# Kernel optimization log

Measured on AMD Instinct MI355X. Metric: run time of the kernel, lower is better.

The kernel has to match this reference:

```python
import jax, jax.numpy as jnp
import numpy as np

LN_EPS = 1e-5


def _layernorm(h, gamma, beta):
    mu = jnp.mean(h, axis=-1, keepdims=True)
    var = jnp.var(h, axis=-1, keepdims=True)
    return (h - mu) * jax.lax.rsqrt(var + LN_EPS) * gamma + beta


def _simple_attention(q, k, v):
    # DIFFormer 'simple' kernel, num_heads=1: global-Frobenius-normalized q,k,
    # linear attention numerator + uniform component, denominator + N.
    n = q.shape[0]
    qs = q / jnp.linalg.norm(q)            # [N, M]
    ks = k / jnp.linalg.norm(k)            # [N, M]
    kvs = jnp.einsum('lm,ld->md', ks, v)   # [M, D]
    num = jnp.einsum('nm,md->nd', qs, kvs) + jnp.sum(v, axis=0)  # [N, D]
    den = jnp.einsum('nm,m->n', qs, jnp.sum(ks, axis=0)) + jnp.asarray(n, q.dtype)
    return num / den[:, None]


def reference(x, edge_index, W1, b1, Wq, bq, Wk, bk, gamma, beta, alpha, Wr, br, wgt):
    n = x.shape[0]
    row, col = edge_index[0], edge_index[1]
    # symmetric GCN normalization (degree of destination index, as in DIFFormer)
    deg = jax.ops.segment_sum(jnp.ones_like(col, dtype=x.dtype), col, num_segments=n)
    inv_sqrt = jnp.where(deg > 0, 1.0 / jnp.sqrt(deg), 0.0)
    w_edge = inv_sqrt[col] * inv_sqrt[row]  # [E]

    def gcn_conv(v):
        # out[i] = sum_{e: col[e]==i} w[e] * v[row[e]]
        return jax.ops.segment_sum(w_edge[:, None] * v[row], col, num_segments=n)

    def conv(h):
        q = h @ Wq + bq
        k = h @ Wk + bk
        v = h                              # use_weight=False -> value = source input
        return _simple_attention(q, k, v) + gcn_conv(v)

    R = jax.nn.relu(x @ W1 + b1)           # [N, H]
    Ts = [R]
    for _ in range(3):                      # three calls of the SAME shared conv
        Rn = conv(R)
        R = alpha * Rn + (1.0 - alpha) * R  # residual blend
        R = _layernorm(R, gamma, beta)      # shared LayerNorm
        Ts.append(R)

    # multi-head linear readout + learned weighted sum (dropout = identity in eval)
    res = jnp.stack([Ts[i] @ Wr[i] + br[i] for i in range(4)], axis=0)  # [4, N]
    out = jnp.einsum('i,in->n', wgt, res)[:, None]                       # [N, 1]
    return out


def setup_inputs():
    key = jax.random.key(0)
    ks = jax.random.split(key, 8)
    N, E, F_IN, H = 100000, 3200000, 58, 256
    x = jax.random.normal(ks[0], (N, F_IN), dtype=jnp.float32)
    edge_index = jax.random.randint(ks[1], (2, E), 0, N, dtype=jnp.int32)
    s_in = 1.0 / np.sqrt(F_IN)
    s_h = 1.0 / np.sqrt(H)
    return {
        'x': x,
        'edge_index': edge_index,
        'W1': jax.random.normal(ks[2], (F_IN, H), dtype=jnp.float32) * s_in,
        'b1': jnp.zeros((H,), jnp.float32),
        'Wq': jax.random.normal(ks[3], (H, H), dtype=jnp.float32) * s_h,
        'bq': jnp.zeros((H,), jnp.float32),
        'Wk': jax.random.normal(ks[4], (H, H), dtype=jnp.float32) * s_h,
        'bk': jnp.zeros((H,), jnp.float32),
        'gamma': jnp.ones((H,), jnp.float32),
        'beta': jnp.zeros((H,), jnp.float32),
        'alpha': jnp.float32(0.5),
        'Wr': jax.random.normal(ks[5], (4, H), dtype=jnp.float32) * s_h,
        'br': jnp.zeros((4,), jnp.float32),
        'wgt': jnp.array([0.5, 0.5, 0.5, 0.5], jnp.float32),
    }
```

## Files before the change

### kernel.cpp

```cpp
#include <hip/hip_runtime.h>

#define H 256
#define FIN 58
#define LN_EPS 1e-5f
#define ROWS_PB 544
#define EPB 8192
#define SBW 11

typedef __bf16 bf16x8 __attribute__((ext_vector_type(8)));
typedef float f32x16 __attribute__((ext_vector_type(16)));
typedef float f32x2 __attribute__((ext_vector_type(2)));

union FragU {
  ushort u[8];
  bf16x8 v;
};


__device__ __forceinline__ float wave_sum(float v) {
#pragma unroll
  for (int off = 1; off < 64; off <<= 1) v += __shfl_xor(v, off, 64);
  return v;
}

__device__ __forceinline__ float block_sum(float v, volatile float* red) {
  const int tid = threadIdx.x;
  v = wave_sum(v);
  __syncthreads();
  if ((tid & 63) == 0) red[tid >> 6] = v;
  __syncthreads();
  return red[0] + red[1] + red[2] + red[3];
}

__device__ __forceinline__ ushort f2bf(float f) {
  unsigned u = __float_as_uint(f);
  unsigned r = (u + 0x7FFFu + ((u >> 16) & 1u)) >> 16;
  return (ushort)r;
}

__device__ __forceinline__ float bf2f(ushort u) {
  return __uint_as_float((unsigned)u << 16);
}

#if __has_builtin(__builtin_amdgcn_cvt_pk_fp8_f32) && __has_builtin(__builtin_amdgcn_cvt_pk_f32_fp8)
__device__ __forceinline__ unsigned pack_fp8x4(float a, float b, float c, float d) {
  int v = 0;
  v = __builtin_amdgcn_cvt_pk_fp8_f32(a, b, v, false);
  v = __builtin_amdgcn_cvt_pk_fp8_f32(c, d, v, true);
  return (unsigned)v;
}
__device__ __forceinline__ void unpack_fp8x4_acc(float* acc, unsigned v) {
  f32x2 lo = __builtin_amdgcn_cvt_pk_f32_fp8((int)v, false);
  f32x2 hi = __builtin_amdgcn_cvt_pk_f32_fp8((int)v, true);
  acc[0] += lo[0]; acc[1] += lo[1]; acc[2] += hi[0]; acc[3] += hi[1];
}
#else
__device__ __forceinline__ unsigned char f2e4m3_1(float f) {
  unsigned u = __float_as_uint(f);
  unsigned s = (u >> 31) << 7;
  float a = fabsf(f);
  if (a >= 448.0f) return (unsigned char)(s | 0x7E);
  if (a < 0.0009765625f) return (unsigned char)s;
  int e;
  float m = frexpf(a, &e);
  int E = e - 1 + 7;
  if (E >= 1) {
    int mm = (int)rintf((m * 2.0f - 1.0f) * 8.0f);
    if (mm == 8) { mm = 0; E++; }
    return (unsigned char)(s | (E << 3) | mm);
  }
  int mm = (int)rintf(a * 512.0f);
  if (mm > 7) return (unsigned char)(s | (1 << 3));
  return (unsigned char)(s | mm);
}
__device__ __forceinline__ unsigned pack_fp8x4(float a, float b, float c, float d) {
  return (unsigned)f2e4m3_1(a) | ((unsigned)f2e4m3_1(b) << 8) |
         ((unsigned)f2e4m3_1(c) << 16) | ((unsigned)f2e4m3_1(d) << 24);
}
__device__ __forceinline__ float e4m3f_1(unsigned v) {
  int s = (v >> 7) & 1, E = (v >> 3) & 15, m = v & 7;
  float mag = E ? ldexpf(1.0f + m * 0.125f, E - 7) : ldexpf((float)m, -9);
  return s ? -mag : mag;
}
__device__ __forceinline__ void unpack_fp8x4_acc(float* acc, unsigned v) {
  acc[0] += e4m3f_1(v & 255);
  acc[1] += e4m3f_1((v >> 8) & 255);
  acc[2] += e4m3f_1((v >> 16) & 255);
  acc[3] += e4m3f_1(v >> 24);
}
#endif


__global__ __launch_bounds__(512) void k_b1(const int* __restrict__ row,
                                            const int* __restrict__ col,
                                            unsigned* __restrict__ breg,
                                            int* __restrict__ gcnt,
                                            int cap2, int E, int nsb) {
  __shared__ unsigned stage[EPB];
  __shared__ int lh[65], lbase[65], lcur[64], gclaim[64];
  const int tid = threadIdx.x;
  const int e0 = blockIdx.x * EPB;
  const int cnt = min(EPB, E - e0);
  if (tid < 64) lh[tid] = 0;
  __syncthreads();
  for (int i = tid; i < cnt; i += 512) atomicAdd(&lh[col[e0 + i] >> SBW], 1);
  __syncthreads();
  if (tid == 0) {
    int acc = 0;
    for (int b = 0; b < nsb; b++) { lbase[b] = acc; acc += lh[b]; }
    lbase[nsb] = acc;
  }
  __syncthreads();
  if (tid < nsb) {
    gclaim[tid] = atomicAdd(&gcnt[tid], lh[tid]);
    lcur[tid] = lbase[tid];
  }
  __syncthreads();
  for (int i = tid; i < cnt; i += 512) {
    int c = col[e0 + i];
    int b = c >> SBW;
    int s = atomicAdd(&lcur[b], 1);
    stage[s] = ((unsigned)row[e0 + i] << SBW) | (unsigned)(c & ((1 << SBW) - 1));
  }
  __syncthreads();
  for (int i = tid; i < cnt; i += 512) {
    int lo = 0, hi = nsb;
    while (hi - lo > 1) {
      int mid = (lo + hi) >> 1;
      if (lbase[mid] <= i) lo = mid; else hi = mid;
    }
    int off = gclaim[lo] + (i - lbase[lo]);
    if (off < cap2) breg[(size_t)lo * cap2 + off] = stage[i];
  }
}

__global__ __launch_bounds__(512) void k_degB2(const unsigned* __restrict__ breg,
                                               const int* __restrict__ gcnt, int cap2,
                                               int* __restrict__ deg, int N) {
  __shared__ int lcnt[1 << SBW];
  const int b = blockIdx.x, tid = threadIdx.x, base = b << SBW;
  for (int i = tid; i < (1 << SBW); i += 512) lcnt[i] = 0;
  __syncthreads();
  const int cnt = min(gcnt[b], cap2);
  const unsigned* p = breg + (size_t)b * cap2;
  for (int i = tid; i < cnt; i += 512) atomicAdd(&lcnt[p[i] & ((1 << SBW) - 1)], 1);
  __syncthreads();
  for (int i = tid; i < (1 << SBW); i += 512) {
    int d = base + i;
    if (d < N) deg[d] = lcnt[i];
  }
}

__global__ __launch_bounds__(512) void k_b2(const unsigned* __restrict__ breg,
                                            const int* __restrict__ gcnt, int cap2,
                                            const int* __restrict__ offs16,
                                            int* __restrict__ eb, int N) {
  __shared__ int loffs[1 << SBW];
  __shared__ int lcur[1 << SBW];
  const int b = blockIdx.x, tid = threadIdx.x, base = b << SBW;
  for (int i = tid; i < (1 << SBW); i += 512) {
    int d = base + i;
    loffs[i] = (d < N) ? offs16[d] : 0;
    lcur[i] = 0;
  }
  __syncthreads();
  const int cnt = min(gcnt[b], cap2);
  const unsigned* p = breg + (size_t)b * cap2;
  for (int i = tid; i < cnt; i += 512) {
    unsigned rc = p[i];
    int lc = rc & ((1 << SBW) - 1);
    int slot = atomicAdd(&lcur[lc], 1);
    eb[loffs[lc] + slot] = (int)(rc >> SBW);
  }
  __syncthreads();
  for (int i = tid; i < (1 << SBW); i += 512) {
    int d = base + i;
    if (d < N) {
      int c = lcur[i];
      int pad = (c + 15) & ~15;
      int o = loffs[i];
      for (int j = c; j < pad; j++) eb[o + j] = N;
    }
  }
}

__global__ void k_invsqrt(const int* __restrict__ deg, float* __restrict__ invs, int N) {
  int i = blockIdx.x * 256 + threadIdx.x;
  if (i < N) {
    int d = deg[i];
    invs[i] = (d > 0) ? (1.0f / sqrtf((float)d)) : 0.0f;
  }
}

__global__ __launch_bounds__(1024) void k_scan1(const int* __restrict__ deg,
                                                int* __restrict__ offs16,
                                                int* __restrict__ bsum, int N) {
  __shared__ int buf[1024];
  const int tid = threadIdx.x;
  const int gid = blockIdx.x * 1024 + tid;
  int v = (gid < N) ? ((deg[gid] + 15) & ~15) : 0;
  buf[tid] = v;
  __syncthreads();
  for (int off = 1; off < 1024; off <<= 1) {
    int x = (tid >= off) ? buf[tid - off] : 0;
    __syncthreads();
    buf[tid] += x;
    __syncthreads();
  }
  if (gid < N) offs16[gid] = buf[tid] - v;
  if (tid == 1023) bsum[blockIdx.x] = buf[1023];
}

__global__ __launch_bounds__(1024) void k_scan2(int* __restrict__ bsum, int nb) {
  __shared__ int buf[1024];
  const int tid = threadIdx.x;
  int v = (tid < nb) ? bsum[tid] : 0;
  buf[tid] = v;
  __syncthreads();
  for (int off = 1; off < 1024; off <<= 1) {
    int x = (tid >= off) ? buf[tid - off] : 0;
    __syncthreads();
    buf[tid] += x;
    __syncthreads();
  }
  if (tid < nb) bsum[tid] = buf[tid] - v;
}

__global__ void k_scan3(int* __restrict__ offs16, const int* __restrict__ bsum, int N) {
  int i = blockIdx.x * 256 + threadIdx.x;
  if (i < N) offs16[i] += bsum[i >> 10];
}

__global__ void k_tofp8(const ushort* __restrict__ Rb, const float* __restrict__ invs,
                        unsigned* __restrict__ Rf8, int total8) {
  for (int i = blockIdx.x * 256 + threadIdx.x; i < total8; i += gridDim.x * 256) {
    float s = invs[i >> 5];
    int4 v = ((const int4*)Rb)[i];
    const ushort* pu = (const ushort*)&v;
    unsigned lo = pack_fp8x4(bf2f(pu[0]) * s, bf2f(pu[1]) * s, bf2f(pu[2]) * s, bf2f(pu[3]) * s);
    unsigned hi = pack_fp8x4(bf2f(pu[4]) * s, bf2f(pu[5]) * s, bf2f(pu[6]) * s, bf2f(pu[7]) * s);
    ((uint2*)Rf8)[i] = make_uint2(lo, hi);
  }
}

__global__ void k_prep(const float* __restrict__ Wq, const float* __restrict__ Wk,
                       const float* __restrict__ bq, const float* __restrict__ bk,
                       float* __restrict__ P, float* __restrict__ Q, float* __restrict__ K2,
                       float* __restrict__ pb, float* __restrict__ qb,
                       float* __restrict__ wb, float* __restrict__ kb,
                       float* __restrict__ sconst) {
  __shared__ float red[4];
  const int b = blockIdx.x, tid = threadIdx.x;
  if (b < 768) {
    const int f = b & 255, which = b >> 8;
    const float* A = (which == 2) ? Wk : Wq;
    const float* Bm = (which == 1) ? Wq : Wk;
    float acc = 0.0f;
    for (int m = 0; m < H; m++) acc = fmaf(A[f * H + m], Bm[tid * H + m], acc);
    float* D = (which == 0) ? P : ((which == 1) ? Q : K2);
    D[f * H + tid] = acc;
  } else {
    float a1 = 0, a2 = 0, a3 = 0, a4 = 0;
    for (int m = 0; m < H; m++) {
      float wqv = Wq[tid * H + m], wkv = Wk[tid * H + m];
      a1 = fmaf(wqv, bk[m], a1);
      a2 = fmaf(wqv, bq[m], a2);
      a3 = fmaf(wkv, bq[m], a3);
      a4 = fmaf(wkv, bk[m], a4);
    }
    pb[tid] = a1; qb[tid] = a2; wb[tid] = a3; kb[tid] = a4;
    float c0 = block_sum(bq[tid] * bk[tid], red);
    float c1 = block_sum(bq[tid] * bq[tid], red);
    float c2 = block_sum(bk[tid] * bk[tid], red);
    if (tid == 0) { sconst[0] = c0; sconst[1] = c1; sconst[2] = c2; }
  }
}

__global__ void k_fc1(const float* __restrict__ x, const float* __restrict__ W1,
                      const float* __restrict__ b1, const float* __restrict__ Wr,
                      const float* __restrict__ br, const float* __restrict__ wgt,
                      ushort* __restrict__ R0, float* __restrict__ out, int N) {
  __shared__ __align__(16) float lx[16 * FIN];
  __shared__ float red2[4][16];
  const int tid = threadIdx.x;
  const int n0 = blockIdx.x * 16;
  for (int idx = tid; idx < 16 * FIN / 4; idx += 256)
    ((float4*)lx)[idx] = ((const float4*)(x + (size_t)n0 * FIN))[idx];
  __syncthreads();
  float acc[16];
  const float bias = b1[tid];
#pragma unroll
  for (int r = 0; r < 16; r++) acc[r] = bias;
  for (int f = 0; f < FIN; f++) {
    float wv = W1[f * H + tid];
#pragma unroll
    for (int r = 0; r < 16; r++) acc[r] = fmaf(lx[r * FIN + f], wv, acc[r]);
  }
  const float wr0 = Wr[tid];
#pragma unroll
  for (int r = 0; r < 16; r++) {
    acc[r] = fmaxf(acc[r], 0.0f);
    int n = n0 + r;
    if (n < N) R0[(size_t)n * H + tid] = f2bf(acc[r]);
  }
#pragma unroll
  for (int r = 0; r < 16; r++) {
    float s = wave_sum(acc[r] * wr0);
    if ((tid & 63) == 0) red2[tid >> 6][r] = s;
  }
  __syncthreads();
  if (tid < 16) {
    int n = n0 + tid;
    if (n < N)
      out[n] = wgt[0] * (red2[0][tid] + red2[1][tid] + red2[2][tid] + red2[3][tid] + br[0]);
  }
}

__global__ __launch_bounds__(512, 2) void k_Gm(const ushort* __restrict__ Rb,
                                               float* __restrict__ Gslab,
                                               float* __restrict__ vsum, int N) {
  __shared__ ushort sb[2][32 * 256];
  const int tid = threadIdx.x;
  const int lane = tid & 63;
  const int wid = tid >> 6;
  const int wrow = (wid & 1) * 128;
  const int wcol = (wid >> 1) * 64;
  const int l31 = lane & 31;
  const int lhi = lane >> 5;

  const int rowbase = blockIdx.x * ROWS_PB;
  const int nrows = min(ROWS_PB, N - rowbase);
  const int nch = (nrows + 31) >> 5;

  const int sk = tid >> 4;
  const int c0 = (tid & 15) * 16;

  f32x16 acc[4][2];
#pragma unroll
  for (int s = 0; s < 4; s++)
#pragma unroll
    for (int t = 0; t < 2; t++)
#pragma unroll
      for (int e = 0; e < 16; e++) acc[s][t][e] = 0.0f;

  float csum[16];
#pragma unroll
  for (int i = 0; i < 16; i++) csum[i] = 0.0f;

  int4 ld[2];

  auto load_chunk = [&](int ch) {
    int g = rowbase + ch * 32 + sk;
    const int4* src = (const int4*)(Rb + (size_t)g * H + c0);
    ld[0] = (g < N) ? src[0] : make_int4(0, 0, 0, 0);
    ld[1] = (g < N) ? src[1] : make_int4(0, 0, 0, 0);
  };

  auto write_chunk = [&](int buf) {
    const int swz = (sk & 3) << 4;
#pragma unroll
    for (int i = 0; i < 2; i++) {
      *(int4*)&sb[buf][sk * 256 + ((c0 + 8 * i) ^ swz)] = ld[i];
      const ushort* pu = (const ushort*)&ld[i];
#pragma unroll
      for (int j = 0; j < 8; j++) csum[8 * i + j] += bf2f(pu[j]);
    }
  };

  auto compute = [&](int buf) {
#pragma unroll
    for (int ks = 0; ks < 2; ks++) {
      const int kb = ks * 16 + lhi * 8;
      FragU fr[6];
#pragma unroll
      for (int s = 0; s < 6; s++) {
        const int cbase = (s < 4) ? (wrow + 32 * s + l31) : (wcol + 32 * (s - 4) + l31);
#pragma unroll
        for (int j = 0; j < 8; j++)
          fr[s].u[j] = sb[buf][(kb + j) * 256 + (cbase ^ ((j & 3) << 4))];
      }
#pragma unroll
      for (int s = 0; s < 4; s++)
#pragma unroll
        for (int t = 0; t < 2; t++)
          acc[s][t] = __builtin_amdgcn_mfma_f32_32x32x16_bf16(fr[s].v, fr[4 + t].v,
                                                              acc[s][t], 0, 0, 0);
    }
  };

  if (nch > 0) {
    load_chunk(0);
    write_chunk(0);
    __syncthreads();
    int cur = 0;
    for (int c = 0; c < nch; c++) {
      if (c + 1 < nch) load_chunk(c + 1);
      compute(cur);
      if (c + 1 < nch) write_chunk(cur ^ 1);
      __syncthreads();
      cur ^= 1;
    }
  }

  float* Gs = Gslab + (size_t)blockIdx.x * 65536;
#pragma unroll
  for (int s = 0; s < 4; s++)
#pragma unroll
    for (int t = 0; t < 2; t++) {
      const int n0 = wcol + 32 * t + l31;
#pragma unroll
      for (int r = 0; r < 16; r++) {
        const int row = wrow + 32 * s + (r & 3) + 8 * (r >> 2) + 4 * lhi;
        Gs[row * 256 + n0] = acc[s][t][r];
      }
    }

  float* fl = (float*)sb;
#pragma unroll
  for (int j = 0; j < 16; j++) fl[sk * 256 + c0 + j] = csum[j];
  __syncthreads();
  if (tid < 256) {
    float s = 0.0f;
    for (int r = 0; r < 32; r++) s += fl[r * 256 + tid];
    atomicAdd(&vsum[tid], s);
  }
}

__global__ void k_Gr(const float* __restrict__ Gslab, float* __restrict__ G, int nslab) {
  const int i = blockIdx.x * 256 + threadIdx.x;
  float s0 = 0, s1 = 0, s2 = 0, s3 = 0;
  int b = 0;
  for (; b + 3 < nslab; b += 4) {
    s0 += Gslab[(size_t)b * 65536 + i];
    s1 += Gslab[(size_t)(b + 1) * 65536 + i];
    s2 += Gslab[(size_t)(b + 2) * 65536 + i];
    s3 += Gslab[(size_t)(b + 3) * 65536 + i];
  }
  float s = s0 + s1 + s2 + s3;
  for (; b < nslab; b++) s += Gslab[(size_t)b * 65536 + i];
  G[i] = s;
}

__global__ void k_small(const float* __restrict__ G, const float* __restrict__ vsum,
                        const float* __restrict__ P, const float* __restrict__ pb,
                        const float* __restrict__ wb, const float* __restrict__ sconst,
                        const float* __restrict__ Q, const float* __restrict__ K2,
                        ushort* __restrict__ Mt, float* __restrict__ cvec,
                        float* __restrict__ dvec, float* __restrict__ scal, int N) {
  __shared__ float red[4];
  const int b = blockIdx.x, tid = threadIdx.x;
  if (b < 256) {
    float acc = 0.0f;
    for (int m = 0; m < H; m++) acc = fmaf(P[b * H + m], G[m * H + tid], acc);
    Mt[(size_t)tid * H + b] = f2bf(acc + pb[b] * vsum[tid]);
  } else if (b == 256) {
    float acc = 0.0f;
    for (int f = 0; f < H; f++) acc = fmaf(wb[f], G[f * H + tid], acc);
    cvec[tid] = acc + sconst[0] * vsum[tid];
  } else if (b == 257) {
    float acc = 0.0f;
    for (int m = 0; m < H; m++) acc = fmaf(P[tid * H + m], vsum[m], acc);
    dvec[tid] = acc + (float)N * pb[tid];
  } else if (b < 274) {
    int base = (b - 258) * 4096 + tid;
    float a = 0.0f;
    for (int j = 0; j < 16; j++) a = fmaf(G[base + j * 256], Q[base + j * 256], a);
    a = block_sum(a, red);
    if (tid == 0) atomicAdd(&scal[0], a);
  } else {
    int base = (b - 274) * 4096 + tid;
    float a = 0.0f;
    for (int j = 0; j < 16; j++) a = fmaf(G[base + j * 256], K2[base + j * 256], a);
    a = block_sum(a, red);
    if (tid == 0) atomicAdd(&scal[1], a);
  }
}

__global__ void k_final(const float* __restrict__ vsum, const float* __restrict__ qb,
                        const float* __restrict__ kb, const float* __restrict__ wb,
                        const float* __restrict__ sconst, float* __restrict__ scal, int N) {
  __shared__ float red[4];
  const int tid = threadIdx.x;
  float s1 = block_sum(qb[tid] * vsum[tid], red);
  float s2 = block_sum(kb[tid] * vsum[tid], red);
  float s3 = block_sum(wb[tid] * vsum[tid], red);
  if (tid == 0) {
    float sq = scal[0] + 2.0f * s1 + (float)N * sconst[1];
    float sk = scal[1] + 2.0f * s2 + (float)N * sconst[2];
    scal[2] = 1.0f / (sqrtf(sq) * sqrtf(sk));
    scal[3] = s3 + (float)N * sconst[0];
  }
}

__global__ __launch_bounds__(512) void k_N(const ushort* __restrict__ Rb,
                                           const ushort* __restrict__ Mt,
                                           ushort* __restrict__ numb, int N) {
  const int tid = threadIdx.x;
  const int lane = tid & 63;
  const int wid = tid >> 6;
  const int l31 = lane & 31;
  const int lhi = lane >> 5;
  const int wrow = (wid & 3) * 32;
  const int wcol = (wid >> 2) * 128;
  const int rowbase = blockIdx.x * 128;

  f32x16 acc[4];
#pragma unroll
  for (int t = 0; t < 4; t++)
#pragma unroll
    for (int e = 0; e < 16; e++) acc[t][e] = 0.0f;

  const ushort* aptr = Rb + (size_t)(rowbase + wrow + l31) * H;

  for (int kc = 0; kc < 16; kc++) {
    const int kb = kc * 16 + lhi * 8;
    FragU fa;
    *(int4*)fa.u = *(const int4*)(aptr + kb);
    FragU fb0, fb1, fb2, fb3;
    *(int4*)fb0.u = *(const int4*)(Mt + (size_t)(wcol + 0 + l31) * H + kb);
    *(int4*)fb1.u = *(const int4*)(Mt + (size_t)(wcol + 32 + l31) * H + kb);
    *(int4*)fb2.u = *(const int4*)(Mt + (size_t)(wcol + 64 + l31) * H + kb);
    *(int4*)fb3.u = *(const int4*)(Mt + (size_t)(wcol + 96 + l31) * H + kb);
    acc[0] = __builtin_amdgcn_mfma_f32_32x32x16_bf16(fa.v, fb0.v, acc[0], 0, 0, 0);
    acc[1] = __builtin_amdgcn_mfma_f32_32x32x16_bf16(fa.v, fb1.v, acc[1], 0, 0, 0);
    acc[2] = __builtin_amdgcn_mfma_f32_32x32x16_bf16(fa.v, fb2.v, acc[2], 0, 0, 0);
    acc[3] = __builtin_amdgcn_mfma_f32_32x32x16_bf16(fa.v, fb3.v, acc[3], 0, 0, 0);
  }

#pragma unroll
  for (int t = 0; t < 4; t++) {
    const int col = wcol + 32 * t + l31;
#pragma unroll
    for (int r = 0; r < 16; r++) {
      const int row = rowbase + wrow + (r & 3) + 8 * (r >> 2) + 4 * lhi;
      if (row < N) numb[(size_t)row * H + col] = f2bf(acc[t][r]);
    }
  }
}

__global__ __launch_bounds__(256) void k_C(
    const ushort* __restrict__ Rb, ushort* __restrict__ Rnext,
    const ushort* __restrict__ numb, const unsigned* __restrict__ Rf8,
    const int* __restrict__ eb, const float* __restrict__ invs,
    const float* __restrict__ cvec, const float* __restrict__ dvec,
    const float* __restrict__ vsum, const float* __restrict__ scal,
    const int* __restrict__ offs16, const int* __restrict__ deg,
    const float* __restrict__ alphap, const float* __restrict__ gamma,
    const float* __restrict__ beta, const float* __restrict__ Wr,
    const float* __restrict__ br, const float* __restrict__ wgt,
    float* __restrict__ out, int N, int layer, int last) {
  const int tid = threadIdx.x, lane = tid & 63, wv = tid >> 6;
  const int d0 = lane * 4;
  const int n0 = blockIdx.x * 32 + wv * 8;

  const float invn = scal[2], denc = scal[3];
  const float al = alphap[0], om = 1.0f - al;
  const float4 dv = *(const float4*)&dvec[d0];
  const float4 cv = *(const float4*)&cvec[d0];
  const float4 vs = *(const float4*)&vsum[d0];
  const float4 gm = *(const float4*)&gamma[d0];
  const float4 bt = *(const float4*)&beta[d0];
  const float4 wr = *(const float4*)&Wr[layer * H + d0];
  const float wl = wgt[layer], bl = br[layer];

  for (int r = 0; r < 8; r++) {
    const int n = n0 + r;
    if (n >= N) break;
    const ushort4 ro = *(const ushort4*)&Rb[(size_t)n * H + d0];
    const ushort4 no = *(const ushort4*)&numb[(size_t)n * H + d0];
    const float old0 = bf2f(ro.x), old1 = bf2f(ro.y), old2 = bf2f(ro.z), old3 = bf2f(ro.w);

    float p = old0 * dv.x + old1 * dv.y + old2 * dv.z + old3 * dv.w;
    p = wave_sum(p);
    const float rden = 1.0f / ((p + denc) * invn + (float)N);

    float a[4] = {0.0f, 0.0f, 0.0f, 0.0f};
    const int st = offs16[n];
    const int nb = (deg[n] + 15) >> 4;
    const int4* pe = (const int4*)(eb + st);
    for (int b = 0; b < nb; b++, pe += 4) {
      int4 q0 = pe[0], q1 = pe[1], q2 = pe[2], q3 = pe[3];
      unsigned g[16];
      g[0] = Rf8[((size_t)q0.x << 6) + lane];
      g[1] = Rf8[((size_t)q0.y << 6) + lane];
      g[2] = Rf8[((size_t)q0.z << 6) + lane];
      g[3] = Rf8[((size_t)q0.w << 6) + lane];
      g[4] = Rf8[((size_t)q1.x << 6) + lane];
      g[5] = Rf8[((size_t)q1.y << 6) + lane];
      g[6] = Rf8[((size_t)q1.z << 6) + lane];
      g[7] = Rf8[((size_t)q1.w << 6) + lane];
      g[8] = Rf8[((size_t)q2.x << 6) + lane];
      g[9] = Rf8[((size_t)q2.y << 6) + lane];
      g[10] = Rf8[((size_t)q2.z << 6) + lane];
      g[11] = Rf8[((size_t)q2.w << 6) + lane];
      g[12] = Rf8[((size_t)q3.x << 6) + lane];
      g[13] = Rf8[((size_t)q3.y << 6) + lane];
      g[14] = Rf8[((size_t)q3.z << 6) + lane];
      g[15] = Rf8[((size_t)q3.w << 6) + lane];
#pragma unroll
      for (int i = 0; i < 16; i++) unpack_fp8x4_acc(a, g[i]);
    }
    const float sn = invs[n];

    float hv0 = al * (((bf2f(no.x) + cv.x) * invn + vs.x) * rden + a[0] * sn) + om * old0;
    float hv1 = al * (((bf2f(no.y) + cv.y) * invn + vs.y) * rden + a[1] * sn) + om * old1;
    float hv2 = al * (((bf2f(no.z) + cv.z) * invn + vs.z) * rden + a[2] * sn) + om * old2;
    float hv3 = al * (((bf2f(no.w) + cv.w) * invn + vs.w) * rden + a[3] * sn) + om * old3;

    float s = wave_sum(hv0 + hv1 + hv2 + hv3);
    float mu = s * (1.0f / H);
    float s2 = wave_sum(hv0 * hv0 + hv1 * hv1 + hv2 * hv2 + hv3 * hv3);
    float var = s2 * (1.0f / H) - mu * mu;
    float rs = rsqrtf(var + LN_EPS);
    float y0 = (hv0 - mu) * rs * gm.x + bt.x;
    float y1 = (hv1 - mu) * rs * gm.y + bt.y;
    float y2 = (hv2 - mu) * rs * gm.z + bt.z;
    float y3 = (hv3 - mu) * rs * gm.w + bt.w;
    if (!last) {
      ushort4 o;
      o.x = f2bf(y0); o.y = f2bf(y1); o.z = f2bf(y2); o.w = f2bf(y3);
      *(ushort4*)&Rnext[(size_t)n * H + d0] = o;
    }
    float rp = wave_sum(y0 * wr.x + y1 * wr.y + y2 * wr.z + y3 * wr.w);
    if (lane == 0) out[n] += wl * (rp + bl);
  }
}


extern "C" void kernel_launch(void* const* d_in, const int* in_sizes, int n_in,
                              void* d_out, int out_size, void* d_ws, size_t ws_size,
                              hipStream_t stream) {
  const float* x = (const float*)d_in[0];
  const int* ei = (const int*)d_in[1];
  const float* W1 = (const float*)d_in[2];
  const float* b1 = (const float*)d_in[3];
  const float* Wq = (const float*)d_in[4];
  const float* bq = (const float*)d_in[5];
  const float* Wk = (const float*)d_in[6];
  const float* bk = (const float*)d_in[7];
  const float* gamma = (const float*)d_in[8];
  const float* beta = (const float*)d_in[9];
  const float* alphap = (const float*)d_in[10];
  const float* Wr = (const float*)d_in[11];
  const float* br = (const float*)d_in[12];
  const float* wgt = (const float*)d_in[13];
  float* out = (float*)d_out;

  const int N = in_sizes[0] / FIN;
  const int E = in_sizes[1] / 2;
  const int* row = ei;
  const int* col = ei + E;

  char* w = (char*)d_ws;
  auto alloc = [&](size_t bytes) -> char* {
    char* p = w;
    w += (bytes + 255) & ~(size_t)255;
    return p;
  };
  const size_t RB = (size_t)(N + 128) * H * sizeof(ushort);
  ushort* Rb0 = (ushort*)alloc(RB);
  ushort* Rb1 = (ushort*)alloc(RB);
  ushort* numb = (ushort*)alloc(RB);
  unsigned* Rf8 = (unsigned*)alloc((size_t)(N + 1) * 64 * sizeof(unsigned));
  ushort* Mt = (ushort*)alloc(H * H * sizeof(ushort));
  float* G = (float*)alloc(H * H * sizeof(float));
  float* vsum = (float*)alloc(1024);
  float* scal = (float*)alloc(256);
  float* cvec = (float*)alloc(1024);
  float* dvec = (float*)alloc(1024);
  float* P = (float*)alloc(H * H * sizeof(float));
  float* Q = (float*)alloc(H * H * sizeof(float));
  float* K2 = (float*)alloc(H * H * sizeof(float));
  float* pb = (float*)alloc(1024);
  float* qb = (float*)alloc(1024);
  float* wb = (float*)alloc(1024);
  float* kb = (float*)alloc(1024);
  float* sconst = (float*)alloc(256);
  int* deg = (int*)alloc((size_t)N * 4);
  float* invs = (float*)alloc((size_t)N * 4);
  int* offs16 = (int*)alloc((size_t)(N + 1) * 4);
  int* bsum = (int*)alloc(1024 * 4);
  int* gcnt = (int*)alloc(64 * 4);
  size_t EPAD = (size_t)E + 16 * (size_t)N;
  EPAD = (EPAD + 3) & ~(size_t)3;
  int* eb = (int*)alloc(EPAD * sizeof(int));

  const int NSB = (N + (1 << SBW) - 1) >> SBW;
  int cap2 = (E / (NSB > 0 ? NSB : 1)) * 2 + 4096;
  cap2 = (cap2 + 3) & ~3;
  unsigned* breg = (unsigned*)Rb1;
  float* Gslab = (float*)numb;

  hipMemsetAsync(gcnt, 0, 64 * 4, stream);
  hipMemsetAsync(Rf8 + (size_t)N * 64, 0, 64 * sizeof(unsigned), stream);

  const int gN = (N + 255) / 256;
  const int nblk = (N + 1023) / 1024;
  const int nbB1 = (E + EPB - 1) / EPB;
  k_b1<<<nbB1, 512, 0, stream>>>(row, col, breg, gcnt, cap2, E, NSB);
  k_degB2<<<NSB, 512, 0, stream>>>(breg, gcnt, cap2, deg, N);
  k_invsqrt<<<gN, 256, 0, stream>>>(deg, invs, N);
  k_scan1<<<nblk, 1024, 0, stream>>>(deg, offs16, bsum, N);
  k_scan2<<<1, 1024, 0, stream>>>(bsum, nblk);
  k_scan3<<<gN, 256, 0, stream>>>(offs16, bsum, N);
  k_b2<<<NSB, 512, 0, stream>>>(breg, gcnt, cap2, offs16, eb, N);
  k_prep<<<769, 256, 0, stream>>>(Wq, Wk, bq, bk, P, Q, K2, pb, qb, wb, kb, sconst);
  const int gRows16 = (N + 15) / 16;
  k_fc1<<<gRows16, 256, 0, stream>>>(x, W1, b1, Wr, br, wgt, Rb0, out, N);

  const int nbG = (N + ROWS_PB - 1) / ROWS_PB;
  const int nbN = (N + 127) / 128;
  const int gRows32 = (N + 31) / 32;
  const int total8 = N * (H / 8);
  ushort* Rc = Rb0;
  ushort* Rn = Rb1;
  for (int it = 1; it <= 3; ++it) {
    hipMemsetAsync(vsum, 0, 1024 + 256, stream);
    k_Gm<<<nbG, 512, 0, stream>>>(Rc, Gslab, vsum, N);
    k_Gr<<<256, 256, 0, stream>>>(Gslab, G, nbG);
    k_small<<<290, 256, 0, stream>>>(G, vsum, P, pb, wb, sconst, Q, K2, Mt, cvec, dvec, scal, N);
    k_final<<<1, 256, 0, stream>>>(vsum, qb, kb, wb, sconst, scal, N);
    k_tofp8<<<2048, 256, 0, stream>>>(Rc, invs, Rf8, total8);
    k_N<<<nbN, 512, 0, stream>>>(Rc, Mt, numb, N);
    k_C<<<gRows32, 256, 0, stream>>>(Rc, Rn, numb, Rf8, eb, invs, cvec, dvec, vsum, scal,
                                     offs16, deg, alphap, gamma, beta, Wr, br, wgt, out,
                                     N, it, (it == 3) ? 1 : 0);
    ushort* t = Rc; Rc = Rn; Rn = t;
  }
}
```

Before: 1.248 ms.

## Fuse fp8 conversion into Gram kernel, store bf16 slabs, widen gather per lane

Removes the separate fp8 conversion kernel by packing the scaled fp8 copy of R inside k_Gm while the chunk is already in registers. Partial Gram slabs are stored as bf16 instead of fp32, halving the slab traffic read by k_Gr, and ROWS_PB drops so more blocks (and slabs) are launched. The combine kernel now processes two rows per wave with 8 features per lane and 8-byte gathers, halving reduction width. Bf16 partial Gram sums lose precision, and the larger slab count adds reduction work.

```diff
diff --git a/kernel.cpp b/kernel.cpp
--- a/kernel.cpp
+++ b/kernel.cpp
@@ -3,7 +3,7 @@
 #define H 256
 #define FIN 58
 #define LN_EPS 1e-5f
-#define ROWS_PB 544
+#define ROWS_PB 384
 #define EPB 8192
 #define SBW 11
 
@@ -20,6 +20,12 @@
 __device__ __forceinline__ float wave_sum(float v) {
 #pragma unroll
   for (int off = 1; off < 64; off <<= 1) v += __shfl_xor(v, off, 64);
+  return v;
+}
+
+__device__ __forceinline__ float half_sum(float v) {
+#pragma unroll
+  for (int off = 1; off < 32; off <<= 1) v += __shfl_xor(v, off, 64);
   return v;
 }
 
@@ -49,10 +55,9 @@
   v = __builtin_amdgcn_cvt_pk_fp8_f32(c, d, v, true);
   return (unsigned)v;
 }
-__device__ __forceinline__ void unpack_fp8x4_acc(float* acc, unsigned v) {
-  f32x2 lo = __builtin_amdgcn_cvt_pk_f32_fp8((int)v, false);
-  f32x2 hi = __builtin_amdgcn_cvt_pk_f32_fp8((int)v, true);
-  acc[0] += lo[0]; acc[1] += lo[1]; acc[2] += hi[0]; acc[3] += hi[1];
+__device__ __forceinline__ void unpack_fp8x2_acc(f32x2& lo, f32x2& hi, unsigned v) {
+  lo += __builtin_amdgcn_cvt_pk_f32_fp8((int)v, false);
+  hi += __builtin_amdgcn_cvt_pk_f32_fp8((int)v, true);
 }
 #else
 __device__ __forceinline__ unsigned char f2e4m3_1(float f) {
@@ -82,11 +87,11 @@
   float mag = E ? ldexpf(1.0f + m * 0.125f, E - 7) : ldexpf((float)m, -9);
   return s ? -mag : mag;
 }
-__device__ __forceinline__ void unpack_fp8x4_acc(float* acc, unsigned v) {
-  acc[0] += e4m3f_1(v & 255);
-  acc[1] += e4m3f_1((v >> 8) & 255);
-  acc[2] += e4m3f_1((v >> 16) & 255);
-  acc[3] += e4m3f_1(v >> 24);
+__device__ __forceinline__ void unpack_fp8x2_acc(f32x2& lo, f32x2& hi, unsigned v) {
+  lo[0] += e4m3f_1(v & 255);
+  lo[1] += e4m3f_1((v >> 8) & 255);
+  hi[0] += e4m3f_1((v >> 16) & 255);
+  hi[1] += e4m3f_1(v >> 24);
 }
 #endif
 
@@ -229,18 +234,6 @@
 __global__ void k_scan3(int* __restrict__ offs16, const int* __restrict__ bsum, int N) {
   int i = blockIdx.x * 256 + threadIdx.x;
   if (i < N) offs16[i] += bsum[i >> 10];
-}
-
-__global__ void k_tofp8(const ushort* __restrict__ Rb, const float* __restrict__ invs,
-                        unsigned* __restrict__ Rf8, int total8) {
-  for (int i = blockIdx.x * 256 + threadIdx.x; i < total8; i += gridDim.x * 256) {
-    float s = invs[i >> 5];
-    int4 v = ((const int4*)Rb)[i];
-    const ushort* pu = (const ushort*)&v;
-    unsigned lo = pack_fp8x4(bf2f(pu[0]) * s, bf2f(pu[1]) * s, bf2f(pu[2]) * s, bf2f(pu[3]) * s);
-    unsigned hi = pack_fp8x4(bf2f(pu[4]) * s, bf2f(pu[5]) * s, bf2f(pu[6]) * s, bf2f(pu[7]) * s);
-    ((uint2*)Rf8)[i] = make_uint2(lo, hi);
-  }
 }
 
 __global__ void k_prep(const float* __restrict__ Wq, const float* __restrict__ Wk,
@@ -317,7 +310,9 @@
 }
 
 __global__ __launch_bounds__(512, 2) void k_Gm(const ushort* __restrict__ Rb,
-                                               float* __restrict__ Gslab,
+                                               const float* __restrict__ invs,
+                                               ushort* __restrict__ Gslab,
+                                               unsigned* __restrict__ Rf8,
                                                float* __restrict__ vsum, int N) {
   __shared__ ushort sb[2][32 * 256];
   const int tid = threadIdx.x;
@@ -356,15 +351,24 @@
     ld[1] = (g < N) ? src[1] : make_int4(0, 0, 0, 0);
   };
 
-  auto write_chunk = [&](int buf) {
+  auto write_chunk = [&](int ch, int buf) {
+    int g = rowbase + ch * 32 + sk;
     const int swz = (sk & 3) << 4;
+    const float sc = (g < N) ? invs[g] : 0.0f;
+    unsigned w8[4];
 #pragma unroll
     for (int i = 0; i < 2; i++) {
       *(int4*)&sb[buf][sk * 256 + ((c0 + 8 * i) ^ swz)] = ld[i];
       const ushort* pu = (const ushort*)&ld[i];
 #pragma unroll
       for (int j = 0; j < 8; j++) csum[8 * i + j] += bf2f(pu[j]);
-    }
+      w8[2 * i] = pack_fp8x4(bf2f(pu[0]) * sc, bf2f(pu[1]) * sc,
+                             bf2f(pu[2]) * sc, bf2f(pu[3]) * sc);
+      w8[2 * i + 1] = pack_fp8x4(bf2f(pu[4]) * sc, bf2f(pu[5]) * sc,
+                                 bf2f(pu[6]) * sc, bf2f(pu[7]) * sc);
+    }
+    if (g < N)
+      *(uint4*)&Rf8[(size_t)g * 64 + (c0 >> 2)] = make_uint4(w8[0], w8[1], w8[2], w8[3]);
   };
 
   auto compute = [&](int buf) {
@@ -390,28 +394,28 @@
 
   if (nch > 0) {
     load_chunk(0);
-    write_chunk(0);
+    write_chunk(0, 0);
     __syncthreads();
     int cur = 0;
     for (int c = 0; c < nch; c++) {
       if (c + 1 < nch) load_chunk(c + 1);
       compute(cur);
-      if (c + 1 < nch) write_chunk(cur ^ 1);
+      if (c + 1 < nch) write_chunk(c + 1, cur ^ 1);
       __syncthreads();
       cur ^= 1;
     }
   }
 
-  float* Gs = Gslab + (size_t)blockIdx.x * 65536;
+  ushort* Gs = Gslab + (size_t)blockIdx.x * 65536;
 #pragma unroll
   for (int s = 0; s < 4; s++)
 #pragma unroll
     for (int t = 0; t < 2; t++) {
-      const int n0 = wcol + 32 * t + l31;
+      const int n0c = wcol + 32 * t + l31;
 #pragma unroll
       for (int r = 0; r < 16; r++) {
         const int row = wrow + 32 * s + (r & 3) + 8 * (r >> 2) + 4 * lhi;
-        Gs[row * 256 + n0] = acc[s][t][r];
+        Gs[row * 256 + n0c] = f2bf(acc[s][t][r]);
       }
     }
 
@@ -426,18 +430,18 @@
   }
 }
 
-__global__ void k_Gr(const float* __restrict__ Gslab, float* __restrict__ G, int nslab) {
+__global__ void k_Gr(const ushort* __restrict__ Gslab, float* __restrict__ G, int nslab) {
   const int i = blockIdx.x * 256 + threadIdx.x;
   float s0 = 0, s1 = 0, s2 = 0, s3 = 0;
   int b = 0;
   for (; b + 3 < nslab; b += 4) {
-    s0 += Gslab[(size_t)b * 65536 + i];
-    s1 += Gslab[(size_t)(b + 1) * 65536 + i];
-    s2 += Gslab[(size_t)(b + 2) * 65536 + i];
-    s3 += Gslab[(size_t)(b + 3) * 65536 + i];
+    s0 += bf2f(Gslab[(size_t)b * 65536 + i]);
+    s1 += bf2f(Gslab[(size_t)(b + 1) * 65536 + i]);
+    s2 += bf2f(Gslab[(size_t)(b + 2) * 65536 + i]);
+    s3 += bf2f(Gslab[(size_t)(b + 3) * 65536 + i]);
   }
   float s = s0 + s1 + s2 + s3;
-  for (; b < nslab; b++) s += Gslab[(size_t)b * 65536 + i];
+  for (; b < nslab; b++) s += bf2f(Gslab[(size_t)b * 65536 + i]);
   G[i] = s;
 }
 
@@ -550,79 +554,97 @@
     const float* __restrict__ br, const float* __restrict__ wgt,
     float* __restrict__ out, int N, int layer, int last) {
   const int tid = threadIdx.x, lane = tid & 63, wv = tid >> 6;
-  const int d0 = lane * 4;
+  const int half = lane >> 5, hl = lane & 31;
+  const int d0 = hl * 8;
   const int n0 = blockIdx.x * 32 + wv * 8;
 
   const float invn = scal[2], denc = scal[3];
   const float al = alphap[0], om = 1.0f - al;
-  const float4 dv = *(const float4*)&dvec[d0];
-  const float4 cv = *(const float4*)&cvec[d0];
-  const float4 vs = *(const float4*)&vsum[d0];
-  const float4 gm = *(const float4*)&gamma[d0];
-  const float4 bt = *(const float4*)&beta[d0];
-  const float4 wr = *(const float4*)&Wr[layer * H + d0];
+  const float4 dvA = *(const float4*)&dvec[d0];
+  const float4 dvB = *(const float4*)&dvec[d0 + 4];
+  const float4 cvA = *(const float4*)&cvec[d0];
+  const float4 cvB = *(const float4*)&cvec[d0 + 4];
+  const float4 vsA = *(const float4*)&vsum[d0];
+  const float4 vsB = *(const float4*)&vsum[d0 + 4];
+  const float4 gmA = *(const float4*)&gamma[d0];
+  const float4 gmB = *(const float4*)&gamma[d0 + 4];
+  const float4 btA = *(const float4*)&beta[d0];
+  const float4 btB = *(const float4*)&beta[d0 + 4];
+  const float4 wrA = *(const float4*)&Wr[layer * H + d0];
+  const float4 wrB = *(const float4*)&Wr[layer * H + d0 + 4];
   const float wl = wgt[layer], bl = br[layer];
 
-  for (int r = 0; r < 8; r++) {
-    const int n = n0 + r;
-    if (n >= N) break;
-    const ushort4 ro = *(const ushort4*)&Rb[(size_t)n * H + d0];
-    const ushort4 no = *(const ushort4*)&numb[(size_t)n * H + d0];
-    const float old0 = bf2f(ro.x), old1 = bf2f(ro.y), old2 = bf2f(ro.z), old3 = bf2f(ro.w);
-
-    float p = old0 * dv.x + old1 * dv.y + old2 * dv.z + old3 * dv.w;
-    p = wave_sum(p);
+  for (int r = 0; r < 4; r++) {
+    const int n = n0 + r * 2 + half;
+    const bool valid = n < N;
+    const int ns = valid ? n : 0;
+
+    const int4 rv = *(const int4*)&Rb[(size_t)ns * H + d0];
+    const int4 nv = *(const int4*)&numb[(size_t)ns * H + d0];
+    const ushort* rp = (const ushort*)&rv;
+    const ushort* np = (const ushort*)&nv;
+    float old[8], num[8];
+#pragma unroll
+    for (int j = 0; j < 8; j++) { old[j] = bf2f(rp[j]); num[j] = bf2f(np[j]); }
+
+    float p = old[0] * dvA.x + old[1] * dvA.y + old[2] * dvA.z + old[3] * dvA.w +
+              old[4] * dvB.x + old[5] * dvB.y + old[6] * dvB.z + old[7] * dvB.w;
+    p = half_sum(p);
     const float rden = 1.0f / ((p + denc) * invn + (float)N);
 
-    float a[4] = {0.0f, 0.0f, 0.0f, 0.0f};
-    const int st = offs16[n];
-    const int nb = (deg[n] + 15) >> 4;
+    f32x2 a01 = {0.f, 0.f}, a23 = {0.f, 0.f}, a45 = {0.f, 0.f}, a67 = {0.f, 0.f};
+    const int st = offs16[ns];
+    const int nbch = valid ? ((deg[ns] + 15) >> 4) : 0;
     const int4* pe = (const int4*)(eb + st);
-    for (int b = 0; b < nb; b++, pe += 4) {
+    const int woff = hl * 2;
+    for (int b = 0; b < nbch; b++, pe += 4) {
       int4 q0 = pe[0], q1 = pe[1], q2 = pe[2], q3 = pe[3];
-      unsigned g[16];
-      g[0] = Rf8[((size_t)q0.x << 6) + lane];
-      g[1] = Rf8[((size_t)q0.y << 6) + lane];
-      g[2] = Rf8[((size_t)q0.z << 6) + lane];
-      g[3] = Rf8[((size_t)q0.w << 6) + lane];
-      g[4] = Rf8[((size_t)q1.x << 6) + lane];
-      g[5] = Rf8[((size_t)q1.y << 6) + lane];
-      g[6] = Rf8[((size_t)q1.z << 6) + lane];
-      g[7] = Rf8[((size_t)q1.w << 6) + lane];
-      g[8] = Rf8[((size_t)q2.x << 6) + lane];
-      g[9] = Rf8[((size_t)q2.y << 6) + lane];
-      g[10] = Rf8[((size_t)q2.z << 6) + lane];
-      g[11] = Rf8[((size_t)q2.w << 6) + lane];
-      g[12] = Rf8[((size_t)q3.x << 6) + lane];
-      g[13] = Rf8[((size_t)q3.y << 6) + lane];
-      g[14] = Rf8[((size_t)q3.z << 6) + lane];
-      g[15] = Rf8[((size_t)q3.w << 6) + lane];
-#pragma unroll
-      for (int i = 0; i < 16; i++) unpack_fp8x4_acc(a, g[i]);
-    }
-    const float sn = invs[n];
-
-    float hv0 = al * (((bf2f(no.x) + cv.x) * invn + vs.x) * rden + a[0] * sn) + om * old0;
-    float hv1 = al * (((bf2f(no.y) + cv.y) * invn + vs.y) * rden + a[1] * sn) + om * old1;
-    float hv2 = al * (((bf2f(no.z) + cv.z) * invn + vs.z) * rden + a[2] * sn) + om * old2;
-    float hv3 = al * (((bf2f(no.w) + cv.w) * invn + vs.w) * rden + a[3] * sn) + om * old3;
-
-    float s = wave_sum(hv0 + hv1 + hv2 + hv3);
-    float mu = s * (1.0f / H);
-    float s2 = wave_sum(hv0 * hv0 + hv1 * hv1 + hv2 * hv2 + hv3 * hv3);
-    float var = s2 * (1.0f / H) - mu * mu;
-    float rs = rsqrtf(var + LN_EPS);
-    float y0 = (hv0 - mu) * rs * gm.x + bt.x;
-    float y1 = (hv1 - mu) * rs * gm.y + bt.y;
-    float y2 = (hv2 - mu) * rs * gm.z + bt.z;
-    float y3 = (hv3 - mu) * rs * gm.w + bt.w;
-    if (!last) {
-      ushort4 o;
-      o.x = f2bf(y0); o.y = f2bf(y1); o.z = f2bf(y2); o.w = f2bf(y3);
-      *(ushort4*)&Rnext[(size_t)n * H + d0] = o;
-    }
-    float rp = wave_sum(y0 * wr.x + y1 * wr.y + y2 * wr.z + y3 * wr.w);
-    if (lane == 0) out[n] += wl * (rp + bl);
+      const int srcs[16] = {q0.x, q0.y, q0.z, q0.w, q1.x, q1.y, q1.z, q1.w,
+                            q2.x, q2.y, q2.z, q2.w, q3.x, q3.y, q3.z, q3.w};
+      uint2 g[16];
+#pragma unroll
+      for (int i = 0; i < 16; i++)
+        g[i] = *(const uint2*)&Rf8[((size_t)srcs[i] << 6) + woff];
+#pragma unroll
+      for (int i = 0; i < 16; i++) {
+        unpack_fp8x2_acc(a01, a23, g[i].x);
+        unpack_fp8x2_acc(a45, a67, g[i].y);
+      }
+    }
+    const float sn = invs[ns];
+    float ag[8] = {a01[0] * sn, a01[1] * sn, a23[0] * sn, a23[1] * sn,
+                   a45[0] * sn, a45[1] * sn, a67[0] * sn, a67[1] * sn};
+
+    const float cva[8] = {cvA.x, cvA.y, cvA.z, cvA.w, cvB.x, cvB.y, cvB.z, cvB.w};
+    const float vsa[8] = {vsA.x, vsA.y, vsA.z, vsA.w, vsB.x, vsB.y, vsB.z, vsB.w};
+    float hv[8];
+#pragma unroll
+    for (int j = 0; j < 8; j++)
+      hv[j] = al * (((num[j] + cva[j]) * invn + vsa[j]) * rden + ag[j]) + om * old[j];
+
+    float s = 0.0f, s2 = 0.0f;
+#pragma unroll
+    for (int j = 0; j < 8; j++) { s += hv[j]; s2 += hv[j] * hv[j]; }
+    s = half_sum(s);
+    s2 = half_sum(s2);
+    const float mu = s * (1.0f / H);
+    const float var = s2 * (1.0f / H) - mu * mu;
+    const float rs = rsqrtf(var + LN_EPS);
+
+    const float gma[8] = {gmA.x, gmA.y, gmA.z, gmA.w, gmB.x, gmB.y, gmB.z, gmB.w};
+    const float bta[8] = {btA.x, btA.y, btA.z, btA.w, btB.x, btB.y, btB.z, btB.w};
+    const float wra[8] = {wrA.x, wrA.y, wrA.z, wrA.w, wrB.x, wrB.y, wrB.z, wrB.w};
+    float y[8], rp2 = 0.0f;
+    ushort yo[8];
+#pragma unroll
+    for (int j = 0; j < 8; j++) {
+      y[j] = (hv[j] - mu) * rs * gma[j] + bta[j];
+      yo[j] = f2bf(y[j]);
+      rp2 += y[j] * wra[j];
+    }
+    if (!last && valid) *(int4*)&Rnext[(size_t)n * H + d0] = *(int4*)yo;
+    rp2 = half_sum(rp2);
+    if (hl == 0 && valid) out[n] += wl * (rp2 + bl);
   }
 }
 
@@ -689,7 +711,7 @@
   int cap2 = (E / (NSB > 0 ? NSB : 1)) * 2 + 4096;
   cap2 = (cap2 + 3) & ~3;
   unsigned* breg = (unsigned*)Rb1;
-  float* Gslab = (float*)numb;
+  ushort* Gslab = (ushort*)numb;
 
   hipMemsetAsync(gcnt, 0, 64 * 4, stream);
   hipMemsetAsync(Rf8 + (size_t)N * 64, 0, 64 * sizeof(unsigned), stream);
@@ -711,16 +733,14 @@
   const int nbG = (N + ROWS_PB - 1) / ROWS_PB;
   const int nbN = (N + 127) / 128;
   const int gRows32 = (N + 31) / 32;
-  const int total8 = N * (H / 8);
   ushort* Rc = Rb0;
   ushort* Rn = Rb1;
   for (int it = 1; it <= 3; ++it) {
     hipMemsetAsync(vsum, 0, 1024 + 256, stream);
-    k_Gm<<<nbG, 512, 0, stream>>>(Rc, Gslab, vsum, N);
+    k_Gm<<<nbG, 512, 0, stream>>>(Rc, invs, Gslab, Rf8, vsum, N);
     k_Gr<<<256, 256, 0, stream>>>(Gslab, G, nbG);
     k_small<<<290, 256, 0, stream>>>(G, vsum, P, pb, wb, sconst, Q, K2, Mt, cvec, dvec, scal, N);
     k_final<<<1, 256, 0, stream>>>(vsum, qb, kb, wb, sconst, scal, N);
-    k_tofp8<<<2048, 256, 0, stream>>>(Rc, invs, Rf8, total8);
     k_N<<<nbN, 512, 0, stream>>>(Rc, Mt, numb, N);
     k_C<<<gRows32, 256, 0, stream>>>(Rc, Rn, numb, Rf8, eb, invs, cvec, dvec, vsum, scal,
                                      offs16, deg, alphap, gamma, beta, Wr, br, wgt, out,
```

After: 1.212 ms. -2.8%, faster.
